# Optimization experiments

Measured on AMD Instinct MI355X. Metric: run time of the kernel, lower is better.

Reference implementation:

```python
import jax, jax.numpy as jnp
import numpy as np

EPS = 1e-12  # torch F.normalize default eps


def setup_inputs() -> dict:
    key = jax.random.key(0)
    ks = jax.random.split(key, 5)
    b, c, h, w = 2, 192, 256, 256
    x = jax.random.normal(ks[0], (b, c, h, w), dtype=jnp.float32)
    temperature = jnp.ones((1, 1, 1), dtype=jnp.float32)
    qkv_w = jax.random.normal(ks[1], (3 * c, c), dtype=jnp.float32) * 0.02
    qkv_b = jax.random.normal(ks[2], (3 * c,), dtype=jnp.float32) * 0.02
    proj_w = jax.random.normal(ks[3], (c, c), dtype=jnp.float32) * 0.02
    proj_b = jax.random.normal(ks[4], (c,), dtype=jnp.float32) * 0.02
    return {"x": x, "temperature": temperature, "qkv_w": qkv_w, "qkv_b": qkv_b,
            "proj_w": proj_w, "proj_b": proj_b}


def reference(x, temperature, qkv_w, qkv_b, proj_w, proj_b):
    b, c, h, w = x.shape
    n = h * w
    # [b, c, h, w] -> [b, n, c] tokens over spatial, features = channels
    xt = x.reshape(b, c, n).transpose(0, 2, 1)
    qkv = xt @ qkv_w.T + qkv_b                     # [b, n, 3c]
    q, k, v = jnp.split(qkv, 3, axis=-1)           # each [b, n, c]
    q = q.transpose(0, 2, 1)                       # [b, c, n]
    k = k.transpose(0, 2, 1)
    v = v.transpose(0, 2, 1)
    # L2 normalize along spatial (last) dim, torch-style clamp
    q = q / jnp.maximum(jnp.linalg.norm(q, axis=-1, keepdims=True), EPS)
    k = k / jnp.maximum(jnp.linalg.norm(k, axis=-1, keepdims=True), EPS)
    attn = jnp.einsum('bcn,bdn->bcd', q, k) * temperature[0, 0, 0]  # [b, c, c]
    attn = jax.nn.softmax(attn, axis=-1)
    out = jnp.einsum('bcd,bdn->bcn', attn, v)      # [b, c, n]
    out = out.reshape(b, c, h, w)
    # 1x1 conv projection = channel matmul
    out = jnp.einsum('bchw,dc->bdhw', out, proj_w) + proj_b[None, :, None, None]
    return out
```

## Files before the change

### kernel.cpp

```cpp
#include <hip/hip_runtime.h>
#include <hip/hip_bf16.h>
#include <stdint.h>

typedef __attribute__((ext_vector_type(8))) __bf16 bf16x8;
typedef __attribute__((ext_vector_type(4))) float f32x4;
typedef __attribute__((ext_vector_type(4))) uint u32x4;

#define C192 192
#define NSP 65536
#define EPS_N 1e-12f

#define SLICE_ELEMS 20224
#define ONES_OFF_E 19968

__device__ __forceinline__ uint32_t f2bf1(float a){
  uint32_t u = __float_as_uint(a);
  return (u + 0x7fffu + ((u >> 16) & 1u)) >> 16;
}
__device__ __forceinline__ uint32_t f2bf2(float lo, float hi){
  return f2bf1(lo) | (f2bf1(hi) << 16);
}
__device__ __forceinline__ float bf2f(ushort u){
  return __uint_as_float(((uint32_t)u) << 16);
}

__global__ __launch_bounds__(384, 3) void k_gram(const float* __restrict__ x,
                                                 ushort* __restrict__ gpart){
  __shared__ ushort xs[2][208 * 64];
  char* lb = (char*)&xs[0][0];
  const int tid = threadIdx.x;
  const int lane = tid & 63, wid = tid >> 6;
  const int l15 = lane & 15, hi = lane >> 4;
  const int b = blockIdx.x >> 8, slice = blockIdx.x & 255;
  const int j0 = slice * 256;

  for (int i = tid; i < 2048; i += 384){
    int buf = i >> 10, idx = i & 1023;
    int row = 192 + (idx >> 6), col = idx & 63;
    int byte = buf * 26624 + row * 128 + col * 2;
    byte ^= (row & 7) << 4;
    *(ushort*)(lb + byte) = (idx < 64) ? (ushort)0x3F80 : (ushort)0;
  }

  const int rA = wid, rB = 11 - wid, nA = 13 - rA;
  f32x4 acc[15];
  #pragma unroll
  for (int t = 0; t < 15; t++) acc[t] = (f32x4){0.f, 0.f, 0.f, 0.f};

  const float* xg = x + ((size_t)b * C192) * NSP + j0;

  float4 rf[8];
  auto LOADREGS = [&](int ch){
    #pragma unroll
    for (int q = 0; q < 4; q++){
      int k = wid * 4 + q;
      int row = k * 8 + (lane >> 3);
      int blk = (lane & 7) ^ (lane >> 3);
      const float* src = xg + (size_t)row * NSP + ch * 64 + blk * 8;
      rf[2 * q]     = *(const float4*)(src);
      rf[2 * q + 1] = *(const float4*)(src + 4);
    }
  };
  auto WRITE = [&](int bi){
    #pragma unroll
    for (int q = 0; q < 4; q++){
      uint4 u;
      u.x = f2bf2(rf[2 * q].x,     rf[2 * q].y);
      u.y = f2bf2(rf[2 * q].z,     rf[2 * q].w);
      u.z = f2bf2(rf[2 * q + 1].x, rf[2 * q + 1].y);
      u.w = f2bf2(rf[2 * q + 1].z, rf[2 * q + 1].w);
      int k = wid * 4 + q;
      *(uint4*)(lb + bi * 26624 + k * 1024 + lane * 16) = u;
    }
  };
  auto COMPUTE = [&](int bi){
    const char* base = lb + bi * 26624;
    #pragma unroll
    for (int ks = 0; ks < 2; ks++){
      bf16x8 aA, aB;
      { int byte = (rA * 16 + l15) * 128 + ks * 64 + hi * 16; byte ^= (l15 & 7) << 4;
        aA = *(const bf16x8*)(base + byte); }
      { int byte = (rB * 16 + l15) * 128 + ks * 64 + hi * 16; byte ^= (l15 & 7) << 4;
        aB = *(const bf16x8*)(base + byte); }
      #pragma unroll
      for (int t = 0; t < 15; t++){
        int j = (t < nA) ? (rA + t) : (rB + t - nA);
        int byte = (j * 16 + l15) * 128 + ks * 64 + hi * 16; byte ^= (l15 & 7) << 4;
        bf16x8 bf = *(const bf16x8*)(base + byte);
        acc[t] = __builtin_amdgcn_mfma_f32_16x16x32_bf16((t < nA) ? aA : aB, bf, acc[t], 0, 0, 0);
      }
    }
  };

  LOADREGS(0); WRITE(0); __syncthreads();
  for (int ch = 0; ch < 4; ch++){
    if (ch < 3) LOADREGS(ch + 1);
    COMPUTE(ch & 1);
    if (ch < 3) WRITE((ch + 1) & 1);
    __syncthreads();
  }

  ushort* gp = gpart + (size_t)(b * 256 + slice) * SLICE_ELEMS;
  #pragma unroll
  for (int t = 0; t < 15; t++){
    int i = (t < nA) ? rA : rB;
    int j = (t < nA) ? (rA + t) : (rB + t - nA);
    if (j < 12){
      int F = 12 * i - (i * (i - 1)) / 2 + (j - i);
      ushort* tp = gp + F * 256;
      #pragma unroll
      for (int r = 0; r < 4; r++) tp[(hi * 4 + r) * 16 + l15] = (ushort)f2bf1(acc[t][r]);
    } else if (l15 == 0){
      ushort* tp = gp + ONES_OFF_E + i * 16;
      #pragma unroll
      for (int r = 0; r < 4; r++) tp[hi * 4 + r] = (ushort)f2bf1(acc[t][r]);
    }
  }
}

__global__ __launch_bounds__(1024) void k_reduce(const ushort* __restrict__ gpart,
                                                 float* __restrict__ gaug,
                                                 const float* __restrict__ qkv_w,
                                                 float* __restrict__ wkT){
  int blk = blockIdx.x, tid = threadIdx.x;
  if (blk < 180){
    __shared__ float red[4][256];
    int b = blk / 90, slot = blk % 90;
    int q = tid >> 8, e = tid & 255;
    float sum = 0.f;
    if (slot < 78){
      const ushort* p = gpart + (size_t)(b * 256 + q) * SLICE_ELEMS + slot * 256 + e;
      #pragma unroll 8
      for (int k2 = 0; k2 < 64; k2++) sum += bf2f(p[(size_t)k2 * (4 * SLICE_ELEMS)]);
    } else if (e < 16){
      int i = slot - 78;
      const ushort* p = gpart + (size_t)(b * 256 + q) * SLICE_ELEMS + ONES_OFF_E + i * 16 + e;
      #pragma unroll 8
      for (int k2 = 0; k2 < 64; k2++) sum += bf2f(p[(size_t)k2 * (4 * SLICE_ELEMS)]);
    }
    red[q][e] = sum;
    __syncthreads();
    if (tid < 256){
      float tot = red[0][tid] + red[1][tid] + red[2][tid] + red[3][tid];
      if (slot < 78){
        int i = 0, off = 0;
        while (slot >= off + (12 - i)){ off += 12 - i; i++; }
        int j = i + (slot - off);
        int row = tid >> 4, col = tid & 15;
        int R = i * 16 + row, Cc = j * 16 + col;
        gaug[((size_t)b * C192 + R) * 193 + Cc] = tot;
        gaug[((size_t)b * C192 + Cc) * 193 + R] = tot;
      } else if (tid < 16){
        int i = slot - 78;
        gaug[((size_t)b * C192 + i * 16 + tid) * 193 + 192] = tot;
      }
    }
  } else {
    int idx = (blk - 180) * 1024 + tid;
    if (idx < 36864){
      int d = idx / 192, e = idx % 192;
      wkT[e * 192 + d] = qkv_w[(192 + d) * 192 + e];
    }
  }
}

__global__ __launch_bounds__(256) void k_pr(const float* __restrict__ gaug,
                                            const float* __restrict__ qkv_w,
                                            const float* __restrict__ qkv_b,
                                            float* __restrict__ pr,
                                            float* __restrict__ norms){
  __shared__ float red[4];
  __shared__ float uSh;
  int blk = blockIdx.x, tid = threadIdx.x;
  int b = blk / 384, which = (blk / 192) % 2, c = blk % 192;
  const float* wrow = qkv_w + (which * 192 + c) * 192;
  float acc = 0.f;
  if (tid < 193){
    const float* g = gaug + (size_t)b * C192 * 193 + tid;
    #pragma unroll 4
    for (int e = 0; e < 192; e++) acc += wrow[e] * g[(size_t)e * 193];
    pr[(((size_t)b * 2 + which) * 192 + c) * 193 + tid] = acc;
  }
  if (tid == 192) uSh = acc;
  float v = (tid < 192) ? acc * wrow[tid] : 0.f;
  for (int o = 32; o > 0; o >>= 1) v += __shfl_down(v, o, 64);
  if ((tid & 63) == 0) red[tid >> 6] = v;
  __syncthreads();
  if (tid == 0){
    float s = red[0] + red[1] + red[2] + red[3];
    float bias = qkv_b[which * 192 + c];
    float n2 = s + 2.f * bias * uSh + 65536.f * bias * bias;
    norms[(b * 2 + which) * 192 + c] = fmaxf(sqrtf(fmaxf(n2, 0.f)), EPS_N);
  }
}

__global__ __launch_bounds__(256) void k_attn(const float* __restrict__ pr,
                                              const float* __restrict__ wkT,
                                              const float* __restrict__ norms,
                                              const float* __restrict__ qkv_b,
                                              const float* __restrict__ temperature,
                                              float* __restrict__ attn){
  __shared__ float Pc[193];
  __shared__ float red[4];
  __shared__ float bcast;
  int blk = blockIdx.x, tid = threadIdx.x;
  int b = blk / 192, c = blk % 192;
  if (tid < 193) Pc[tid] = pr[(((size_t)b * 2 + 0) * 192 + c) * 193 + tid];
  __syncthreads();
  int d = tid;
  float logit = -1e30f, p = 0.f;
  if (d < 192){
    float sS = 0.f;
    #pragma unroll 4
    for (int e = 0; e < 192; e++) sS += Pc[e] * wkT[e * 192 + d];
    float bq = qkv_b[c], bk = qkv_b[192 + d];
    float w2 = pr[(((size_t)b * 2 + 1) * 192 + d) * 193 + 192];
    float Sv = sS + Pc[192] * bk + bq * w2 + 65536.f * bq * bk;
    float nq = norms[(b * 2 + 0) * 192 + c];
    float nk = norms[(b * 2 + 1) * 192 + d];
    logit = temperature[0] * Sv / (nq * nk);
  }
  float m = logit;
  for (int o = 32; o > 0; o >>= 1) m = fmaxf(m, __shfl_down(m, o, 64));
  if ((tid & 63) == 0) red[tid >> 6] = m;
  __syncthreads();
  if (tid == 0) bcast = fmaxf(fmaxf(red[0], red[1]), fmaxf(red[2], red[3]));
  __syncthreads();
  m = bcast;
  p = (d < 192) ? __expf(logit - m) : 0.f;
  float s = p;
  for (int o = 32; o > 0; o >>= 1) s += __shfl_down(s, o, 64);
  __syncthreads();
  if ((tid & 63) == 0) red[tid >> 6] = s;
  __syncthreads();
  if (tid == 0) bcast = red[0] + red[1] + red[2] + red[3];
  __syncthreads();
  if (d < 192) attn[((size_t)b * 192 + c) * 192 + d] = p / bcast;
}

__global__ __launch_bounds__(256) void k_u(const float* __restrict__ attn,
                                           const float* __restrict__ qkv_w,
                                           const float* __restrict__ qkv_b,
                                           float* __restrict__ uaug){
  __shared__ float arow[192];
  int blk = blockIdx.x, tid = threadIdx.x;
  int b = blk / 192, c = blk % 192;
  if (tid < 192) arow[tid] = attn[((size_t)b * 192 + c) * 192 + tid];
  __syncthreads();
  int e = tid;
  if (e <= 192){
    float acc = 0.f;
    if (e < 192){
      #pragma unroll 4
      for (int d = 0; d < 192; d++) acc += arow[d] * qkv_w[(384 + d) * 192 + e];
    } else {
      #pragma unroll 4
      for (int d = 0; d < 192; d++) acc += arow[d] * qkv_b[384 + d];
    }
    uaug[((size_t)b * 192 + c) * 193 + e] = acc;
  }
}

__global__ __launch_bounds__(256) void k_f(const float* __restrict__ uaug,
                                           const float* __restrict__ proj_w,
                                           const float* __restrict__ proj_b,
                                           ushort* __restrict__ fb,
                                           float* __restrict__ gvec){
  __shared__ float pw[192];
  int blk = blockIdx.x, tid = threadIdx.x;
  int b = blk / 192, f = blk % 192;
  if (tid < 192) pw[tid] = proj_w[f * 192 + tid];
  __syncthreads();
  int e = tid;
  if (e <= 192){
    float acc = 0.f;
    const float* u = uaug + (size_t)b * 192 * 193 + e;
    #pragma unroll 4
    for (int c2 = 0; c2 < 192; c2++) acc += pw[c2] * u[(size_t)c2 * 193];
    if (e < 192) fb[((size_t)b * 192 + f) * 192 + e] = (ushort)f2bf1(acc);
    else gvec[b * 192 + f] = acc + proj_b[f];
  }
}

__global__ __launch_bounds__(256, 3) void k_out(const float* __restrict__ x,
                                                const ushort* __restrict__ fb,
                                                const float* __restrict__ gvec,
                                                float* __restrict__ out){
  __shared__ ushort xt[128 * 192];
  char* lb = (char*)xt;
  const int tid = threadIdx.x;
  const int lane = tid & 63, wid = tid >> 6;
  const int l15 = lane & 15, hi = lane >> 4;
  const int b = blockIdx.x >> 9, cb = blockIdx.x & 511;
  const int j0 = cb * 128;

  const float* xg = x + ((size_t)b * C192) * NSP + j0;
  #pragma unroll 2
  for (int i = 0; i < 6; i++){
    int unit = i * 256 + tid;
    int cp = unit >> 4, s8 = unit & 15;
    int c0 = cp * 2, sp0 = s8 * 8;
    const float* r0 = xg + (size_t)c0 * NSP + sp0;
    const float* r1 = xg + (size_t)(c0 + 1) * NSP + sp0;
    float4 a0 = *(const float4*)(r0);
    float4 a1 = *(const float4*)(r0 + 4);
    float4 b0 = *(const float4*)(r1);
    float4 b1 = *(const float4*)(r1 + 4);
    float fa[8] = {a0.x, a0.y, a0.z, a0.w, a1.x, a1.y, a1.z, a1.w};
    float fc[8] = {b0.x, b0.y, b0.z, b0.w, b1.x, b1.y, b1.z, b1.w};
    #pragma unroll
    for (int s = 0; s < 8; s++){
      int sp = sp0 + s;
      int byte = sp * 384 + c0 * 2;
      byte ^= (((sp & 7) ^ ((sp >> 3) & 7)) << 4);
      *(uint*)(lb + byte) = f2bf2(fa[s], fc[s]);
    }
  }

  float gfr[3][4];
  #pragma unroll
  for (int i = 0; i < 3; i++)
    #pragma unroll
    for (int r = 0; r < 4; r++)
      gfr[i][r] = gvec[b * 192 + (wid * 3 + i) * 16 + hi * 4 + r];

  f32x4 acc[3][8];
  #pragma unroll
  for (int i = 0; i < 3; i++)
    #pragma unroll
    for (int j = 0; j < 8; j++)
      acc[i][j] = (f32x4){0.f, 0.f, 0.f, 0.f};

  __syncthreads();

  for (int w = 0; w < 6; w++){
    bf16x8 aF[3];
    #pragma unroll
    for (int i = 0; i < 3; i++){
      const ushort* fr = fb + ((size_t)b * 192 + (wid * 3 + i) * 16 + l15) * 192;
      aF[i] = *(const bf16x8*)(fr + w * 32 + hi * 8);
    }
    #pragma unroll
    for (int ct = 0; ct < 8; ct++){
      int sp = ct * 16 + l15;
      int byte = sp * 384 + w * 64 + hi * 16;
      byte ^= (((sp & 7) ^ ((sp >> 3) & 7)) << 4);
      bf16x8 bf = *(const bf16x8*)(lb + byte);
      #pragma unroll
      for (int i = 0; i < 3; i++)
        acc[i][ct] = __builtin_amdgcn_mfma_f32_16x16x32_bf16(aF[i], bf, acc[i][ct], 0, 0, 0);
    }
  }

  #pragma unroll
  for (int i = 0; i < 3; i++){
    int row0 = (wid * 3 + i) * 16 + hi * 4;
    #pragma unroll
    for (int ct = 0; ct < 8; ct++){
      int sp = j0 + ct * 16 + l15;
      float* ob = out + ((size_t)b * C192 + row0) * NSP + sp;
      #pragma unroll
      for (int r = 0; r < 4; r++) ob[(size_t)r * NSP] = acc[i][ct][r] + gfr[i][r];
    }
  }
}

extern "C" void kernel_launch(void* const* d_in, const int* in_sizes, int n_in,
                              void* d_out, int out_size, void* d_ws, size_t ws_size,
                              hipStream_t stream){
  const float* x           = (const float*)d_in[0];
  const float* temperature = (const float*)d_in[1];
  const float* qkv_w       = (const float*)d_in[2];
  const float* qkv_b       = (const float*)d_in[3];
  const float* proj_w      = (const float*)d_in[4];
  const float* proj_b      = (const float*)d_in[5];
  float* out = (float*)d_out;
  char* ws = (char*)d_ws;

  ushort* gpart = (ushort*)(ws);
  float*  gaug  = (float*) (ws + 20709376);
  float*  pr    = (float*) (ws + 21005824);
  float*  wkT   = (float*) (ws + 21598720);
  float*  norms = (float*) (ws + 21746176);
  float*  attn  = (float*) (ws + 21749248);
  float*  uaug  = (float*) (ws + 22044160);
  ushort* fb    = (ushort*)(ws + 22340608);
  float*  gvec  = (float*) (ws + 22488064);

  hipLaunchKernelGGL(k_gram,   dim3(512),  dim3(384),  0, stream, x, gpart);
  hipLaunchKernelGGL(k_reduce, dim3(216),  dim3(1024), 0, stream, gpart, gaug, qkv_w, wkT);
  hipLaunchKernelGGL(k_pr,     dim3(768),  dim3(256),  0, stream, gaug, qkv_w, qkv_b, pr, norms);
  hipLaunchKernelGGL(k_attn,   dim3(384),  dim3(256),  0, stream, pr, wkT, norms, qkv_b, temperature, attn);
  hipLaunchKernelGGL(k_u,      dim3(384),  dim3(256),  0, stream, attn, qkv_w, qkv_b, uaug);
  hipLaunchKernelGGL(k_f,      dim3(384),  dim3(256),  0, stream, uaug, proj_w, proj_b, fb, gvec);
  hipLaunchKernelGGL(k_out,    dim3(1024), dim3(256),  0, stream, x, fb, gvec, out);
}
```

Before: 149.9 us.

## Halve gram slice width, synthesize ones operand in registers, vectorize partial stores

The gram kernel now processes 128-column slices over 1024 blocks instead of 256 over 512, doubling the grid to improve occupancy and latency hiding. The ones row used for row sums is built in registers instead of stored in shared memory, which cuts LDS per block. Partial Gram tiles are written as packed uint2 in MFMA lane order, and the reduce kernel remaps its indices to match. In exchange, the partial buffer doubles in size and the reduce kernel must sum 128 partials instead of 64.

```diff
diff --git a/kernel.cpp b/kernel.cpp
--- a/kernel.cpp
+++ b/kernel.cpp
@@ -26,21 +26,13 @@
 
 __global__ __launch_bounds__(384, 3) void k_gram(const float* __restrict__ x,
                                                  ushort* __restrict__ gpart){
-  __shared__ ushort xs[2][208 * 64];
+  __shared__ ushort xs[2][192 * 64];
   char* lb = (char*)&xs[0][0];
   const int tid = threadIdx.x;
   const int lane = tid & 63, wid = tid >> 6;
   const int l15 = lane & 15, hi = lane >> 4;
-  const int b = blockIdx.x >> 8, slice = blockIdx.x & 255;
-  const int j0 = slice * 256;
-
-  for (int i = tid; i < 2048; i += 384){
-    int buf = i >> 10, idx = i & 1023;
-    int row = 192 + (idx >> 6), col = idx & 63;
-    int byte = buf * 26624 + row * 128 + col * 2;
-    byte ^= (row & 7) << 4;
-    *(ushort*)(lb + byte) = (idx < 64) ? (ushort)0x3F80 : (ushort)0;
-  }
+  const int b = blockIdx.x >> 9, slice = blockIdx.x & 511;
+  const int j0 = slice * 128;
 
   const int rA = wid, rB = 11 - wid, nA = 13 - rA;
   f32x4 acc[15];
@@ -70,11 +62,14 @@
       u.z = f2bf2(rf[2 * q + 1].x, rf[2 * q + 1].y);
       u.w = f2bf2(rf[2 * q + 1].z, rf[2 * q + 1].w);
       int k = wid * 4 + q;
-      *(uint4*)(lb + bi * 26624 + k * 1024 + lane * 16) = u;
+      *(uint4*)(lb + bi * 24576 + k * 1024 + lane * 16) = u;
     }
   };
   auto COMPUTE = [&](int bi){
-    const char* base = lb + bi * 26624;
+    const char* base = lb + bi * 24576;
+    uint ov = (l15 == 0) ? 0x3F803F80u : 0u;
+    u32x4 oq = {ov, ov, ov, ov};
+    bf16x8 onesf = __builtin_bit_cast(bf16x8, oq);
     #pragma unroll
     for (int ks = 0; ks < 2; ks++){
       bf16x8 aA, aB;
@@ -85,35 +80,35 @@
       #pragma unroll
       for (int t = 0; t < 15; t++){
         int j = (t < nA) ? (rA + t) : (rB + t - nA);
-        int byte = (j * 16 + l15) * 128 + ks * 64 + hi * 16; byte ^= (l15 & 7) << 4;
-        bf16x8 bf = *(const bf16x8*)(base + byte);
+        bf16x8 bf;
+        if (j < 12){
+          int byte = (j * 16 + l15) * 128 + ks * 64 + hi * 16; byte ^= (l15 & 7) << 4;
+          bf = *(const bf16x8*)(base + byte);
+        } else {
+          bf = onesf;
+        }
         acc[t] = __builtin_amdgcn_mfma_f32_16x16x32_bf16((t < nA) ? aA : aB, bf, acc[t], 0, 0, 0);
       }
     }
   };
 
   LOADREGS(0); WRITE(0); __syncthreads();
-  for (int ch = 0; ch < 4; ch++){
-    if (ch < 3) LOADREGS(ch + 1);
-    COMPUTE(ch & 1);
-    if (ch < 3) WRITE((ch + 1) & 1);
-    __syncthreads();
-  }
-
-  ushort* gp = gpart + (size_t)(b * 256 + slice) * SLICE_ELEMS;
+  LOADREGS(1); COMPUTE(0); WRITE(1); __syncthreads();
+  COMPUTE(1);
+
+  ushort* gp = gpart + (size_t)(b * 512 + slice) * SLICE_ELEMS;
   #pragma unroll
   for (int t = 0; t < 15; t++){
     int i = (t < nA) ? rA : rB;
     int j = (t < nA) ? (rA + t) : (rB + t - nA);
+    uint2 u2;
+    u2.x = f2bf2(acc[t][0], acc[t][1]);
+    u2.y = f2bf2(acc[t][2], acc[t][3]);
     if (j < 12){
       int F = 12 * i - (i * (i - 1)) / 2 + (j - i);
-      ushort* tp = gp + F * 256;
-      #pragma unroll
-      for (int r = 0; r < 4; r++) tp[(hi * 4 + r) * 16 + l15] = (ushort)f2bf1(acc[t][r]);
+      *(uint2*)(gp + F * 256 + lane * 4) = u2;
     } else if (l15 == 0){
-      ushort* tp = gp + ONES_OFF_E + i * 16;
-      #pragma unroll
-      for (int r = 0; r < 4; r++) tp[hi * 4 + r] = (ushort)f2bf1(acc[t][r]);
+      *(uint2*)(gp + ONES_OFF_E + i * 16 + hi * 4) = u2;
     }
   }
 }
@@ -129,14 +124,14 @@
     int q = tid >> 8, e = tid & 255;
     float sum = 0.f;
     if (slot < 78){
-      const ushort* p = gpart + (size_t)(b * 256 + q) * SLICE_ELEMS + slot * 256 + e;
+      const ushort* p = gpart + (size_t)(b * 512 + q) * SLICE_ELEMS + slot * 256 + e;
       #pragma unroll 8
-      for (int k2 = 0; k2 < 64; k2++) sum += bf2f(p[(size_t)k2 * (4 * SLICE_ELEMS)]);
+      for (int k2 = 0; k2 < 128; k2++) sum += bf2f(p[(size_t)k2 * (4 * SLICE_ELEMS)]);
     } else if (e < 16){
       int i = slot - 78;
-      const ushort* p = gpart + (size_t)(b * 256 + q) * SLICE_ELEMS + ONES_OFF_E + i * 16 + e;
+      const ushort* p = gpart + (size_t)(b * 512 + q) * SLICE_ELEMS + ONES_OFF_E + i * 16 + e;
       #pragma unroll 8
-      for (int k2 = 0; k2 < 64; k2++) sum += bf2f(p[(size_t)k2 * (4 * SLICE_ELEMS)]);
+      for (int k2 = 0; k2 < 128; k2++) sum += bf2f(p[(size_t)k2 * (4 * SLICE_ELEMS)]);
     }
     red[q][e] = sum;
     __syncthreads();
@@ -146,7 +141,9 @@
         int i = 0, off = 0;
         while (slot >= off + (12 - i)){ off += 12 - i; i++; }
         int j = i + (slot - off);
-        int row = tid >> 4, col = tid & 15;
+        int e2 = tid;
+        int row = ((e2 >> 6) << 2) | (e2 & 3);
+        int col = (e2 >> 2) & 15;
         int R = i * 16 + row, Cc = j * 16 + col;
         gaug[((size_t)b * C192 + R) * 193 + Cc] = tot;
         gaug[((size_t)b * C192 + Cc) * 193 + R] = tot;
@@ -378,16 +375,16 @@
   char* ws = (char*)d_ws;
 
   ushort* gpart = (ushort*)(ws);
-  float*  gaug  = (float*) (ws + 20709376);
-  float*  pr    = (float*) (ws + 21005824);
-  float*  wkT   = (float*) (ws + 21598720);
-  float*  norms = (float*) (ws + 21746176);
-  float*  attn  = (float*) (ws + 21749248);
-  float*  uaug  = (float*) (ws + 22044160);
-  ushort* fb    = (ushort*)(ws + 22340608);
-  float*  gvec  = (float*) (ws + 22488064);
-
-  hipLaunchKernelGGL(k_gram,   dim3(512),  dim3(384),  0, stream, x, gpart);
+  float*  gaug  = (float*) (ws + 41418752);
+  float*  pr    = (float*) (ws + 41715200);
+  float*  wkT   = (float*) (ws + 42308096);
+  float*  norms = (float*) (ws + 42455552);
+  float*  attn  = (float*) (ws + 42458624);
+  float*  uaug  = (float*) (ws + 42753536);
+  ushort* fb    = (ushort*)(ws + 43049984);
+  float*  gvec  = (float*) (ws + 43197440);
+
+  hipLaunchKernelGGL(k_gram,   dim3(1024), dim3(384),  0, stream, x, gpart);
   hipLaunchKernelGGL(k_reduce, dim3(216),  dim3(1024), 0, stream, gpart, gaug, qkv_w, wkT);
   hipLaunchKernelGGL(k_pr,     dim3(768),  dim3(256),  0, stream, gaug, qkv_w, qkv_b, pr, norms);
   hipLaunchKernelGGL(k_attn,   dim3(384),  dim3(256),  0, stream, pr, wkT, norms, qkv_b, temperature, attn);
```

Measured after the change: 157.6 us. 5.1% more time.
